# Kernel tuning notes

Measured on AMD Instinct MI355X. Metric: run time of the kernel, lower is better.

The kernel has to match this reference:

```python
import jax, jax.numpy as jnp
import numpy as np

ALPHA = 0.2  # LeakyReLU negative slope
N, IN_DIM, OUT_DIM = 8192, 512, 64


def setup_inputs() -> dict:
    key = jax.random.key(0)
    k1, k2, k3, k4 = jax.random.split(key, 4)
    X = jax.random.normal(k1, (N, IN_DIM), dtype=jnp.float32)
    Adj = jax.random.randint(k2, (N, N), 0, 2, dtype=jnp.int32)
    # xavier_uniform with gain=1.414
    def xavier(k, shape, gain=1.414):
        fan_in, fan_out = shape[0], shape[1]
        bound = gain * np.sqrt(6.0 / (fan_in + fan_out))
        return jax.random.uniform(k, shape, jnp.float32, -bound, bound)
    W = xavier(k3, (IN_DIM, OUT_DIM))
    a = xavier(k4, (2 * OUT_DIM, 1))
    return {"X": X, "Adj": Adj, "W": W, "a": a}


def reference(X, Adj, W, a):
    # h = X @ W : [N, D]
    h = X @ W
    D = h.shape[1]
    # Decompose pairwise score: concat([h_i, h_j]) @ a == h_i @ a1 + h_j @ a2
    s1 = h @ a[:D, 0]   # [N] -- contribution of row (destination) node i
    s2 = h @ a[D:, 0]   # [N] -- contribution of column (source) node j
    e = jnp.exp(jax.nn.leaky_relu(s1[:, None] + s2[None, :], negative_slope=ALPHA))  # [N, N]
    e = jnp.where(Adj == 0, jnp.float32(0.0), e)
    attention = e / jnp.sum(e, axis=1, keepdims=True)
    # dropout is a no-op in eval mode (training=False)
    return attention @ h
```

## Files before the change

kernel.cpp:

```cpp
#include <hip/hip_runtime.h>
#include <math.h>


#define NN 8192
#define KIN 512
#define DD 64
#define ALPHA 0.2f

using floatx4 = __attribute__((ext_vector_type(4))) float;
using bf16x8  = __attribute__((ext_vector_type(8))) __bf16;
using intx4   = __attribute__((ext_vector_type(4))) int;

__global__ __launch_bounds__(256) void k_fused(const float* __restrict__ X,
                                               const float* __restrict__ W,
                                               const float* __restrict__ a,
                                               float* __restrict__ s1,
                                               float* __restrict__ s2,
                                               __bf16* __restrict__ hFrag) {
    __shared__ __align__(16) float smem[3200];
    float* XT = smem;
    float* WL = smem + 32 * 36;
    float* hT = smem;
    const int t = threadIdx.x;
    const int i0 = blockIdx.x * 32;
    const int rb = t >> 5;
    const int db = t & 31;
    float acc[4][2] = {};

    for (int k0 = 0; k0 < KIN; k0 += 32) {
        {
            const int row = t >> 3, kq = t & 7;
            const float4 x4 = *(const float4*)(X + (size_t)(i0 + row) * KIN + k0 + kq * 4);
            XT[(kq * 4 + 0) * 36 + row] = x4.x;
            XT[(kq * 4 + 1) * 36 + row] = x4.y;
            XT[(kq * 4 + 2) * 36 + row] = x4.z;
            XT[(kq * 4 + 3) * 36 + row] = x4.w;
#pragma unroll
            for (int p = 0; p < 2; ++p) {
                const int q = p * 256 + t;
                const int kk = q >> 4, dq = q & 15;
                *(float4*)(WL + kk * 64 + dq * 4) =
                    *(const float4*)(W + (size_t)(k0 + kk) * DD + dq * 4);
            }
        }
        __syncthreads();
#pragma unroll
        for (int k = 0; k < 32; ++k) {
            const float4 xa = *(const float4*)(XT + k * 36 + rb * 4);
            const float2 wb = *(const float2*)(WL + k * 64 + db * 2);
            const float xv[4] = {xa.x, xa.y, xa.z, xa.w};
#pragma unroll
            for (int i = 0; i < 4; ++i) {
                acc[i][0] += xv[i] * wb.x;
                acc[i][1] += xv[i] * wb.y;
            }
        }
        __syncthreads();
    }
#pragma unroll
    for (int i = 0; i < 4; ++i) {
        hT[(rb * 4 + i) * 66 + db * 2 + 0] = acc[i][0];
        hT[(rb * 4 + i) * 66 + db * 2 + 1] = acc[i][1];
    }
    __syncthreads();
    {
        const int r = t >> 3, sub = t & 7;
        float p1 = 0.f, p2 = 0.f;
#pragma unroll
        for (int u = 0; u < 8; ++u) {
            const int d = sub * 8 + u;
            const float v = hT[r * 66 + d];
            p1 += v * a[d];
            p2 += v * a[64 + d];
        }
#pragma unroll
        for (int off = 1; off < 8; off <<= 1) {
            p1 += __shfl_xor(p1, off, 64);
            p2 += __shfl_xor(p2, off, 64);
        }
        if (sub == 0) {
            s1[i0 + r] = p1;
            s2[i0 + r] = p2;
        }
    }
    {
        const int lane = t & 63, dt = t >> 6;
        const int n = lane & 15, q = lane >> 4;
        bf16x8 v;
#pragma unroll
        for (int jj = 0; jj < 8; ++jj)
            v[jj] = (__bf16)hT[(q * 8 + jj) * 66 + dt * 16 + n];
        *(bf16x8*)(hFrag + ((size_t)blockIdx.x * 256 + t) * 8) = v;
    }
}

__global__ __launch_bounds__(256, 4) void k_attn6(const bf16x8* __restrict__ hFrag,
                                                  const int* __restrict__ Adj,
                                                  const float* __restrict__ s1,
                                                  const float* __restrict__ s2,
                                                  float* __restrict__ numP,
                                                  float* __restrict__ denP) {
    const int t = threadIdx.x;
    const int wv = t >> 6;
    const int lane = t & 63;
    const int n = lane & 15, q = lane >> 4;
    const int it = blockIdx.x >> 3, jc = blockIdx.x & 7;
    const int i0 = it * 64;
    const int row = i0 + wv * 16 + n;
    const float s1v = s1[row];
    const int jbase = jc * 1024;
    const int* adjL = Adj + (size_t)row * NN + jbase + q * 8;
    const float* s2L = s2 + jbase + q * 8;
    const bf16x8* hfL = hFrag + (size_t)(jc * 32) * 4 * 64 + lane;

    bf16x8 ones;
#pragma unroll
    for (int u = 0; u < 8; ++u) ones[u] = (__bf16)1.0f;

    floatx4 acc[5] = {};

#pragma unroll 1
    for (int ks = 0; ks < 32; ks += 2) {
        const intx4 a00 = __builtin_nontemporal_load((const intx4*)(adjL + ks * 32));
        const intx4 a01 = __builtin_nontemporal_load((const intx4*)(adjL + ks * 32 + 4));
        const intx4 a10 = __builtin_nontemporal_load((const intx4*)(adjL + ks * 32 + 32));
        const intx4 a11 = __builtin_nontemporal_load((const intx4*)(adjL + ks * 32 + 36));
        const float4 z00 = *(const float4*)(s2L + ks * 32);
        const float4 z01 = *(const float4*)(s2L + ks * 32 + 4);
        const float4 z10 = *(const float4*)(s2L + ks * 32 + 32);
        const float4 z11 = *(const float4*)(s2L + ks * 32 + 36);
#pragma unroll
        for (int sub = 0; sub < 2; ++sub) {
            const intx4 aa = sub ? a10 : a00;
            const intx4 ab = sub ? a11 : a01;
            const float4 za = sub ? z10 : z00;
            const float4 zb = sub ? z11 : z01;
            const int am[8] = {aa.x, aa.y, aa.z, aa.w, ab.x, ab.y, ab.z, ab.w};
            const float zz[8] = {za.x, za.y, za.z, za.w, zb.x, zb.y, zb.z, zb.w};
            bf16x8 af;
#pragma unroll
            for (int u = 0; u < 8; ++u) {
                const float s = s1v + zz[u];
                const float l = fmaxf(s, ALPHA * s);
                const float e = am[u] ? __expf(l) : 0.f;
                af[u] = (__bf16)e;
            }
            const bf16x8* hf = hfL + (size_t)(ks + sub) * 4 * 64;
#pragma unroll
            for (int dt = 0; dt < 4; ++dt)
                acc[dt] = __builtin_amdgcn_mfma_f32_16x16x32_bf16(af, hf[dt * 64], acc[dt], 0, 0, 0);
            acc[4] = __builtin_amdgcn_mfma_f32_16x16x32_bf16(af, ones, acc[4], 0, 0, 0);
        }
    }

    const size_t base = (size_t)blockIdx.x * 4096;
#pragma unroll
    for (int dt = 0; dt < 4; ++dt)
#pragma unroll
        for (int r = 0; r < 4; ++r)
            numP[base + (size_t)(wv * 16 + q * 4 + r) * 64 + dt * 16 + n] = acc[dt][r];

    if (n == 0) {
#pragma unroll
        for (int r = 0; r < 4; ++r)
            denP[(size_t)blockIdx.x * 64 + wv * 16 + q * 4 + r] = acc[4][r];
    }
}

__global__ __launch_bounds__(256) void k_final(const float* __restrict__ numP,
                                               const float* __restrict__ denP,
                                               float* __restrict__ out) {
    const int idx = blockIdx.x * 256 + threadIdx.x;
    const int i = idx >> 6, d = idx & 63;
    const int it = i >> 6, r = i & 63;
    float num = 0.f, den = 0.f;
#pragma unroll
    for (int c = 0; c < 8; ++c) {
        const size_t bx = (size_t)(it * 8 + c);
        num += numP[bx * 4096 + (size_t)r * 64 + d];
        den += denP[bx * 64 + r];
    }
    out[idx] = num / den;
}

extern "C" void kernel_launch(void* const* d_in, const int* in_sizes, int n_in,
                              void* d_out, int out_size, void* d_ws, size_t ws_size,
                              hipStream_t stream) {
    const float* X = (const float*)d_in[0];
    const int* Adj = (const int*)d_in[1];
    const float* W = (const float*)d_in[2];
    const float* a = (const float*)d_in[3];
    float* out = (float*)d_out;

    float* ws = (float*)d_ws;
    float* s1 = ws;
    float* s2 = s1 + 8192;
    __bf16* hFrag = (__bf16*)(s2 + 8192);
    float* numP = (float*)(s2 + 8192 + 262144);
    float* denP = numP + 1024 * 4096;

    k_fused<<<256, 256, 0, stream>>>(X, W, a, s1, s2, hFrag);
    k_attn6<<<1024, 256, 0, stream>>>((const bf16x8*)hFrag, Adj, s1, s2, numP, denP);
    k_final<<<2048, 256, 0, stream>>>(numP, denP, out);
}
```

Baseline: 443.0 us.

## Stage adjacency tiles into LDS via async global_load_lds double buffering

The attention kernel now has each block handle 16 rows across all columns, streaming 512-column adjacency windows into a double-buffered LDS tile with asynchronous global-to-LDS loads. The goal is to overlap adjacency fetches with the exp/MFMA work and to coalesce the row loads. Each wave takes a quarter of every window and writes its own partials, and the final reduction sums four wave partials instead of eight column chunks. The cost is an extra barrier per window, a grid halved to 512 blocks, and about 66KB of LDS per block, which limits occupancy.

Result: faster. 410.9 us (-7.2%).

```diff
diff --git a/kernel.cpp b/kernel.cpp
--- a/kernel.cpp
+++ b/kernel.cpp
@@ -7,9 +7,18 @@
 #define DD 64
 #define ALPHA 0.2f
 
+#define WJ 512
+#define NWIN (NN / WJ)
+#define ASTR 516
+#define ABUF (16 * ASTR)
+
 using floatx4 = __attribute__((ext_vector_type(4))) float;
 using bf16x8  = __attribute__((ext_vector_type(8))) __bf16;
-using intx4   = __attribute__((ext_vector_type(4))) int;
+
+__device__ __forceinline__ void glds16(const int* g, int* l) {
+    __builtin_amdgcn_global_load_lds((const __attribute__((address_space(1))) void*)g,
+                                     (__attribute__((address_space(3))) void*)l, 16, 0, 0);
+}
 
 __global__ __launch_bounds__(256) void k_fused(const float* __restrict__ X,
                                                const float* __restrict__ W,
@@ -94,24 +103,18 @@
     }
 }
 
-__global__ __launch_bounds__(256, 4) void k_attn6(const bf16x8* __restrict__ hFrag,
-                                                  const int* __restrict__ Adj,
-                                                  const float* __restrict__ s1,
-                                                  const float* __restrict__ s2,
-                                                  float* __restrict__ numP,
-                                                  float* __restrict__ denP) {
+__global__ __launch_bounds__(256) void k_attn7(const bf16x8* __restrict__ hFrag,
+                                               const int* __restrict__ Adj,
+                                               const float* __restrict__ s1,
+                                               const float* __restrict__ s2,
+                                               float* __restrict__ numP,
+                                               float* __restrict__ denP) {
+    __shared__ int lds_adj[2 * ABUF];
     const int t = threadIdx.x;
-    const int wv = t >> 6;
-    const int lane = t & 63;
+    const int wv = t >> 6, lane = t & 63;
     const int n = lane & 15, q = lane >> 4;
-    const int it = blockIdx.x >> 3, jc = blockIdx.x & 7;
-    const int i0 = it * 64;
-    const int row = i0 + wv * 16 + n;
-    const float s1v = s1[row];
-    const int jbase = jc * 1024;
-    const int* adjL = Adj + (size_t)row * NN + jbase + q * 8;
-    const float* s2L = s2 + jbase + q * 8;
-    const bf16x8* hfL = hFrag + (size_t)(jc * 32) * 4 * 64 + lane;
+    const int i0 = blockIdx.x * 16;
+    const float s1v = s1[i0 + n];
 
     bf16x8 ones;
 #pragma unroll
@@ -119,24 +122,36 @@
 
     floatx4 acc[5] = {};
 
+    auto issue = [&](int w, int buf) {
+        const int jg0 = w * WJ;
+#pragma unroll
+        for (int r4 = 0; r4 < 4; ++r4) {
+            const int r = wv * 4 + r4;
+            const int* gsrc = Adj + (size_t)(i0 + r) * NN + jg0 + lane * 4;
+            int* ldst = lds_adj + buf * ABUF + r * ASTR;
+            glds16(gsrc, ldst);
+            glds16(gsrc + 256, ldst + 256);
+        }
+    };
+
+    issue(0, 0);
+    issue(1, 1);
+
 #pragma unroll 1
-    for (int ks = 0; ks < 32; ks += 2) {
-        const intx4 a00 = __builtin_nontemporal_load((const intx4*)(adjL + ks * 32));
-        const intx4 a01 = __builtin_nontemporal_load((const intx4*)(adjL + ks * 32 + 4));
-        const intx4 a10 = __builtin_nontemporal_load((const intx4*)(adjL + ks * 32 + 32));
-        const intx4 a11 = __builtin_nontemporal_load((const intx4*)(adjL + ks * 32 + 36));
-        const float4 z00 = *(const float4*)(s2L + ks * 32);
-        const float4 z01 = *(const float4*)(s2L + ks * 32 + 4);
-        const float4 z10 = *(const float4*)(s2L + ks * 32 + 32);
-        const float4 z11 = *(const float4*)(s2L + ks * 32 + 36);
-#pragma unroll
-        for (int sub = 0; sub < 2; ++sub) {
-            const intx4 aa = sub ? a10 : a00;
-            const intx4 ab = sub ? a11 : a01;
-            const float4 za = sub ? z10 : z00;
-            const float4 zb = sub ? z11 : z01;
-            const int am[8] = {aa.x, aa.y, aa.z, aa.w, ab.x, ab.y, ab.z, ab.w};
-            const float zz[8] = {za.x, za.y, za.z, za.w, zb.x, zb.y, zb.z, zb.w};
+    for (int w = 0; w < NWIN; ++w) {
+        const int buf = w & 1;
+        __syncthreads();
+        const int* ldsb = lds_adj + buf * ABUF + n * ASTR;
+#pragma unroll
+        for (int k4 = 0; k4 < 4; ++k4) {
+            const int ks = wv * 4 + k4;
+            const int jg = w * WJ + ks * 32 + q * 8;
+            const float4 z0 = *(const float4*)(s2 + jg);
+            const float4 z1 = *(const float4*)(s2 + jg + 4);
+            const int4 m0 = *(const int4*)(ldsb + ks * 32 + q * 8);
+            const int4 m1 = *(const int4*)(ldsb + ks * 32 + q * 8 + 4);
+            const int am[8] = {m0.x, m0.y, m0.z, m0.w, m1.x, m1.y, m1.z, m1.w};
+            const float zz[8] = {z0.x, z0.y, z0.z, z0.w, z1.x, z1.y, z1.z, z1.w};
             bf16x8 af;
 #pragma unroll
             for (int u = 0; u < 8; ++u) {
@@ -145,25 +160,27 @@
                 const float e = am[u] ? __expf(l) : 0.f;
                 af[u] = (__bf16)e;
             }
-            const bf16x8* hf = hfL + (size_t)(ks + sub) * 4 * 64;
+            const bf16x8* hf = hFrag + (size_t)(w * 16 + ks) * 4 * 64 + lane;
 #pragma unroll
             for (int dt = 0; dt < 4; ++dt)
                 acc[dt] = __builtin_amdgcn_mfma_f32_16x16x32_bf16(af, hf[dt * 64], acc[dt], 0, 0, 0);
             acc[4] = __builtin_amdgcn_mfma_f32_16x16x32_bf16(af, ones, acc[4], 0, 0, 0);
         }
-    }
-
-    const size_t base = (size_t)blockIdx.x * 4096;
+        __syncthreads();
+        if (w + 2 < NWIN) issue(w + 2, buf);
+    }
+
+    const size_t base = ((size_t)blockIdx.x * 4 + wv) * 1024;
 #pragma unroll
     for (int dt = 0; dt < 4; ++dt)
 #pragma unroll
         for (int r = 0; r < 4; ++r)
-            numP[base + (size_t)(wv * 16 + q * 4 + r) * 64 + dt * 16 + n] = acc[dt][r];
+            numP[base + (size_t)(q * 4 + r) * 64 + dt * 16 + n] = acc[dt][r];
 
     if (n == 0) {
 #pragma unroll
         for (int r = 0; r < 4; ++r)
-            denP[(size_t)blockIdx.x * 64 + wv * 16 + q * 4 + r] = acc[4][r];
+            denP[((size_t)blockIdx.x * 4 + wv) * 16 + q * 4 + r] = acc[4][r];
     }
 }
 
@@ -172,13 +189,12 @@
                                                float* __restrict__ out) {
     const int idx = blockIdx.x * 256 + threadIdx.x;
     const int i = idx >> 6, d = idx & 63;
-    const int it = i >> 6, r = i & 63;
+    const int blk = i >> 4, r = i & 15;
     float num = 0.f, den = 0.f;
 #pragma unroll
-    for (int c = 0; c < 8; ++c) {
-        const size_t bx = (size_t)(it * 8 + c);
-        num += numP[bx * 4096 + (size_t)r * 64 + d];
-        den += denP[bx * 64 + r];
+    for (int wv = 0; wv < 4; ++wv) {
+        num += numP[((size_t)blk * 4 + wv) * 1024 + (size_t)r * 64 + d];
+        den += denP[((size_t)blk * 4 + wv) * 16 + r];
     }
     out[idx] = num / den;
 }
@@ -197,9 +213,9 @@
     float* s2 = s1 + 8192;
     __bf16* hFrag = (__bf16*)(s2 + 8192);
     float* numP = (float*)(s2 + 8192 + 262144);
-    float* denP = numP + 1024 * 4096;
+    float* denP = numP + 512 * 4 * 1024;
 
     k_fused<<<256, 256, 0, stream>>>(X, W, a, s1, s2, hFrag);
-    k_attn6<<<1024, 256, 0, stream>>>((const bf16x8*)hFrag, Adj, s1, s2, numP, denP);
+    k_attn7<<<512, 256, 0, stream>>>((const bf16x8*)hFrag, Adj, s1, s2, numP, denP);
     k_final<<<2048, 256, 0, stream>>>(numP, denP, out);
 }
```
